# Kernel optimization log

Hardware: AMD Instinct MI355X
Metric: run time of the kernel (lower is better)

The kernel has to match this reference:

```python
import jax, jax.numpy as jnp
import numpy as np

B, H, W, C = 16, 64, 64, 256
NH = 8
KD = C // NH  # 32
SCALE = KD ** -0.5


def rotate_every_two(x):
    x1 = x[..., ::2]
    x2 = x[..., 1::2]
    return jnp.stack([-x2, x1], axis=-1).reshape(x.shape)


def theta_shift(x, sin, cos):
    return x * cos + rotate_every_two(x) * sin


def dwconv2d(x, w, b):
    # x: (b,h,w,c), w: (5,5,1,c) HWIO depthwise, pad 2
    y = jax.lax.conv_general_dilated(
        x, w, window_strides=(1, 1), padding=((2, 2), (2, 2)),
        dimension_numbers=("NHWC", "HWIO", "NHWC"), feature_group_count=x.shape[-1])
    return y + b


def setup_inputs() -> dict:
    key = jax.random.key(0)
    ks = jax.random.split(key, 12)
    s = 0.02
    return {
        "x": jax.random.normal(ks[0], (B, H, W, C), jnp.float32),
        "sin": jax.random.uniform(ks[1], (H, W, KD), jnp.float32, -1.0, 1.0),
        "cos": jax.random.uniform(ks[2], (H, W, KD), jnp.float32, -1.0, 1.0),
        "mask_h": jax.random.normal(ks[3], (NH, H, H), jnp.float32) * 0.1,
        "mask_w": jax.random.normal(ks[4], (NH, W, W), jnp.float32) * 0.1,
        "Wq": jax.random.normal(ks[5], (C, C), jnp.float32) * s,
        "bq": jnp.zeros((C,), jnp.float32),
        "Wk": jax.random.normal(ks[6], (C, C), jnp.float32) * s,
        "bk": jnp.zeros((C,), jnp.float32),
        "Wv": jax.random.normal(ks[7], (C, C), jnp.float32) * s,
        "bv": jnp.zeros((C,), jnp.float32),
        "conv_w": jax.random.normal(ks[8], (5, 5, 1, C), jnp.float32) * s,
        "conv_b": jnp.zeros((C,), jnp.float32),
        "Wo": jax.random.normal(ks[9], (C, C), jnp.float32) * s,
        "bo": jnp.zeros((C,), jnp.float32),
    }


def reference(x, sin, cos, mask_h, mask_w, Wq, bq, Wk, bk, Wv, bv, conv_w, conv_b, Wo, bo):
    b, h, w, _ = x.shape
    n = mask_w.shape[0]
    kd = sin.shape[-1]

    q = x @ Wq + bq
    k = (x @ Wk + bk) * SCALE
    v = x @ Wv + bv
    lepe = dwconv2d(v, conv_w, conv_b)

    # (b,n,h,w,d)
    q = q.reshape(b, h, w, n, kd).transpose(0, 3, 1, 2, 4)
    k = k.reshape(b, h, w, n, kd).transpose(0, 3, 1, 2, 4)
    qr = theta_shift(q, sin, cos)
    kr = theta_shift(k, sin, cos)

    # width attention: rows independent
    qk_w = jnp.einsum("bhnwd,bhnvd->bhnwv", qr.transpose(0, 2, 1, 3, 4), kr.transpose(0, 2, 1, 3, 4))
    qk_w = jax.nn.softmax(qk_w + mask_w, axis=-1)
    vv = v.reshape(b, h, w, n, -1).transpose(0, 1, 3, 2, 4)  # (b,h,n,w,d2)
    vv = jnp.einsum("bhnwv,bhnvd->bhnwd", qk_w, vv)

    # height attention: columns independent
    qr_h = qr.transpose(0, 3, 1, 2, 4)  # (b,w,n,h,d)
    kr_h = kr.transpose(0, 3, 1, 2, 4)
    vv = vv.transpose(0, 3, 2, 1, 4)  # (b,w,n,h,d2)
    qk_h = jnp.einsum("bwnhd,bwngd->bwnhg", qr_h, kr_h)
    qk_h = jax.nn.softmax(qk_h + mask_h, axis=-1)
    out = jnp.einsum("bwnhg,bwngd->bwnhd", qk_h, vv)

    out = out.transpose(0, 3, 1, 2, 4).reshape(b, h, w, -1)  # (b,h,w,n*d2)
    out = out + lepe
    return out @ Wo + bo
```

## Files before the change

### kernel.cpp

```cpp
#include <hip/hip_runtime.h>

typedef __attribute__((ext_vector_type(8))) short bf16x8;
typedef __attribute__((ext_vector_type(4))) float f32x4;

constexpr int B  = 16;
constexpr int H  = 64;
constexpr int W  = 64;
constexpr int C  = 256;
constexpr int NH = 8;
constexpr int KD = 32;
constexpr float SCALE = 0.17677669529663687f;
constexpr int M_TOT = B * H * W;
constexpr size_t NEL = (size_t)B * H * W * C;

__device__ __forceinline__ unsigned short f2bf(float f) {
    union { float f; unsigned int u; } x; x.f = f;
    unsigned int u = x.u;
    unsigned int r = (u + 0x7fffu + ((u >> 16) & 1u)) >> 16;
    return (unsigned short)r;
}
__device__ __forceinline__ float bf2f(unsigned short s) {
    union { unsigned int u; float f; } x; x.u = ((unsigned int)s) << 16; return x.f;
}
__device__ __forceinline__ float bf_lo(unsigned int u) {
    union { unsigned int u; float f; } x; x.u = u << 16; return x.f;
}
__device__ __forceinline__ float bf_hi(unsigned int u) {
    union { unsigned int u; float f; } x; x.u = u & 0xffff0000u; return x.f;
}
__device__ __forceinline__ unsigned int pack2(float a, float b) {
    return (unsigned int)f2bf(a) | ((unsigned int)f2bf(b) << 16);
}
__device__ __forceinline__ void cvt8(uint4 rv, float* f) {
    f[0] = bf_lo(rv.x); f[1] = bf_hi(rv.x); f[2] = bf_lo(rv.y); f[3] = bf_hi(rv.y);
    f[4] = bf_lo(rv.z); f[5] = bf_hi(rv.z); f[6] = bf_lo(rv.w); f[7] = bf_hi(rv.w);
}
__device__ __forceinline__ int swz(int row, int kp8) {
    return row * 32 + (kp8 ^ (((row >> 2) & 3) << 3));
}

typedef const __attribute__((address_space(1))) unsigned int gas_uint;
typedef __attribute__((address_space(3))) unsigned int las_uint;
__device__ __forceinline__ void gl16(const unsigned short* g, unsigned short* l) {
    __builtin_amdgcn_global_load_lds((gas_uint*)g, (las_uint*)l, 16, 0, 0);
}

__global__ __launch_bounds__(256) void prep_x16(const float* __restrict__ x,
                                                unsigned short* __restrict__ x16) {
    size_t i8 = ((size_t)blockIdx.x * 256 + threadIdx.x) * 8;
    float4 f0 = *(const float4*)(x + i8);
    float4 f1 = *(const float4*)(x + i8 + 4);
    uint4 o;
    o.x = pack2(f0.x, f0.y); o.y = pack2(f0.z, f0.w);
    o.z = pack2(f1.x, f1.y); o.w = pack2(f1.z, f1.w);
    *(uint4*)(x16 + i8) = o;
}

__global__ __launch_bounds__(256) void trans_w(const float* __restrict__ src,
                                               unsigned short* __restrict__ dst) {
    int tid = blockIdx.x * 256 + threadIdx.x;
    int n = tid >> 5, k0 = (tid & 31) << 3;
    unsigned int p[4];
#pragma unroll
    for (int j = 0; j < 4; ++j) {
        float a  = src[(size_t)(k0 + 2 * j) * 256 + n];
        float b2 = src[(size_t)(k0 + 2 * j + 1) * 256 + n];
        p[j] = pack2(a, b2);
    }
    uint4 o = {p[0], p[1], p[2], p[3]};
    *(uint4*)(dst + (size_t)n * 256 + k0) = o;
}

template <int QK>
__global__ __launch_bounds__(256) void qkv_part(
    const unsigned short* __restrict__ x16, const unsigned short* __restrict__ Wt16,
    const float* __restrict__ bq, const float* __restrict__ bk, const float* __restrict__ bv,
    const float* __restrict__ sin_t, const float* __restrict__ cos_t,
    unsigned short* __restrict__ qr, unsigned short* __restrict__ kr,
    unsigned short* __restrict__ v16)
{
    __shared__ __align__(16) unsigned short As[2][128 * 32];
    __shared__ __align__(16) unsigned short Bs[2][128 * 32];

    const int t = threadIdx.x;
    const int lane = t & 63, wid = t >> 6;
    const int wr = wid >> 1, wc = wid & 1;
    const int m0 = blockIdx.x * 128;
    const int yb = blockIdx.y;
    const int wrow0 = QK ? yb * 128 : 512 + yb * 128;
    const int nb    = QK ? (yb & 1) * 128 : yb * 128;
    const int matid = QK ? (yb >> 1) : 2;

    f32x4 acc[4][4];
#pragma unroll
    for (int i = 0; i < 4; ++i)
#pragma unroll
        for (int j = 0; j < 4; ++j)
#pragma unroll
            for (int q = 0; q < 4; ++q) acc[i][j][q] = 0.f;

    const int lco = ((lane >> 2) << 8) + (((lane & 3) ^ (lane >> 4)) << 3);
    const unsigned short* ag = x16 + (size_t)m0 * 256 + lco;
    const unsigned short* bg = Wt16 + (size_t)wrow0 * 256 + lco;
    const int lds0 = wid * 16 * 32;
    const int lds1 = (64 + wid * 16) * 32;
    const int rg0 = wid * 16 * 256, rg1 = (64 + wid * 16) * 256;

    const int rsel = lane & 15, kg8 = (lane >> 4) << 3;

    gl16(ag + rg0, &As[0][lds0]);
    gl16(ag + rg1, &As[0][lds1]);
    gl16(bg + rg0, &Bs[0][lds0]);
    gl16(bg + rg1, &Bs[0][lds1]);
    __syncthreads();

    int cur = 0;
    for (int ks = 0; ks < 8; ++ks) {
        if (ks < 7) {
            const int kn = (ks + 1) * 32;
            gl16(ag + rg0 + kn, &As[cur ^ 1][lds0]);
            gl16(ag + rg1 + kn, &As[cur ^ 1][lds1]);
            gl16(bg + rg0 + kn, &Bs[cur ^ 1][lds0]);
            gl16(bg + rg1 + kn, &Bs[cur ^ 1][lds1]);
        }

        bf16x8 af[4], bf[4];
#pragma unroll
        for (int i = 0; i < 4; ++i)
            af[i] = *(const bf16x8*)(&As[cur][swz(wr * 64 + i * 16 + rsel, kg8)]);
#pragma unroll
        for (int j = 0; j < 4; ++j)
            bf[j] = *(const bf16x8*)(&Bs[cur][swz(wc * 64 + j * 16 + rsel, kg8)]);
#pragma unroll
        for (int i = 0; i < 4; ++i)
#pragma unroll
            for (int j = 0; j < 4; ++j) {
                if (QK)
                    acc[i][j] = __builtin_amdgcn_mfma_f32_16x16x32_bf16(bf[j], af[i], acc[i][j], 0, 0, 0);
                else
                    acc[i][j] = __builtin_amdgcn_mfma_f32_16x16x32_bf16(af[i], bf[j], acc[i][j], 0, 0, 0);
            }
        __syncthreads();
        cur ^= 1;
    }

    const int col_l = lane & 15, rowg = (lane >> 4) << 2;
    if (QK == 0) {
#pragma unroll
        for (int i = 0; i < 4; ++i)
#pragma unroll
            for (int j = 0; j < 4; ++j) {
                int nn = nb + wc * 64 + j * 16 + col_l;
                float bias = bv[nn];
#pragma unroll
                for (int r = 0; r < 4; ++r) {
                    int m = m0 + wr * 64 + i * 16 + rowg + r;
                    v16[(size_t)m * 256 + nn] = f2bf(acc[i][j][r] + bias);
                }
            }
    } else {
        const float sc = matid ? SCALE : 1.0f;
        const float* __restrict__ bias = matid ? bk : bq;
        unsigned short* __restrict__ dst = matid ? kr : qr;
#pragma unroll
        for (int i = 0; i < 4; ++i) {
            const int m = m0 + wr * 64 + i * 16 + col_l;
            const int bb = m >> 12, hh = (m >> 6) & 63, ww = m & 63;
            const size_t pixbase = ((size_t)hh * 64 + ww) * 32;
#pragma unroll
            for (int j = 0; j < 4; ++j) {
                const int n = nb + wc * 64 + j * 16 + rowg;
                const int nh = n >> 5, db = n & 31;
                float4 bias4 = *(const float4*)(bias + n);
                float4 cs4 = *(const float4*)(cos_t + pixbase + db);
                float4 sn4 = *(const float4*)(sin_t + pixbase + db);
                float v0 = (acc[i][j][0] + bias4.x) * sc;
                float v1 = (acc[i][j][1] + bias4.y) * sc;
                float v2 = (acc[i][j][2] + bias4.z) * sc;
                float v3 = (acc[i][j][3] + bias4.w) * sc;
                ushort4 o;
                o.x = f2bf(v0 * cs4.x - v1 * sn4.x);
                o.y = f2bf(v1 * cs4.y + v0 * sn4.y);
                o.z = f2bf(v2 * cs4.z - v3 * sn4.z);
                o.w = f2bf(v3 * cs4.w + v2 * sn4.w);
                *(ushort4*)(dst + ((((size_t)bb * 8 + nh) * 64 + hh) * 64 + ww) * 32 + db) = o;
            }
        }
    }
}

__global__ __launch_bounds__(256) void conv_kernel(
    const unsigned short* __restrict__ v, const float* __restrict__ cw,
    const float* __restrict__ cb, unsigned short* __restrict__ lepe)
{
    size_t tid = (size_t)blockIdx.x * 256 + threadIdx.x;
    const int c8 = (int)(tid & 31) << 3;
    const int w0 = ((int)(tid >> 5) & 15) << 2;
    const int h  = (int)(tid >> 9) & 63;
    const int b  = (int)(tid >> 15);

    float acc[4][8];
    {
        float4 cb0 = *(const float4*)(cb + c8);
        float4 cb1 = *(const float4*)(cb + c8 + 4);
#pragma unroll
        for (int o = 0; o < 4; ++o) {
            acc[o][0] = cb0.x; acc[o][1] = cb0.y; acc[o][2] = cb0.z; acc[o][3] = cb0.w;
            acc[o][4] = cb1.x; acc[o][5] = cb1.y; acc[o][6] = cb1.z; acc[o][7] = cb1.w;
        }
    }

    const unsigned short* __restrict__ vb = v + (size_t)b * 4096 * 256 + c8;
#pragma unroll
    for (int dy = 0; dy < 5; ++dy) {
        const int yy = h + dy - 2;
        if (yy < 0 || yy >= 64) continue;
        float rowf[8][8];
#pragma unroll
        for (int j = 0; j < 8; ++j) {
            const int xx = w0 + j - 2;
            if (xx < 0 || xx >= 64) {
#pragma unroll
                for (int q = 0; q < 8; ++q) rowf[j][q] = 0.f;
            } else {
                uint4 rv = *(const uint4*)(vb + (size_t)(yy * 64 + xx) * 256);
                cvt8(rv, rowf[j]);
            }
        }
#pragma unroll
        for (int dx = 0; dx < 5; ++dx) {
            const float* wp = cw + (dy * 5 + dx) * 256 + c8;
            float4 wv0 = *(const float4*)wp;
            float4 wv1 = *(const float4*)(wp + 4);
#pragma unroll
            for (int o = 0; o < 4; ++o) {
                const float* rf = rowf[dx + o];
                acc[o][0] += rf[0] * wv0.x; acc[o][1] += rf[1] * wv0.y;
                acc[o][2] += rf[2] * wv0.z; acc[o][3] += rf[3] * wv0.w;
                acc[o][4] += rf[4] * wv1.x; acc[o][5] += rf[5] * wv1.y;
                acc[o][6] += rf[6] * wv1.z; acc[o][7] += rf[7] * wv1.w;
            }
        }
    }

    unsigned short* __restrict__ op = lepe + (((size_t)(b * 64 + h) * 64) + w0) * 256 + c8;
#pragma unroll
    for (int o = 0; o < 4; ++o) {
        uint4 ov;
        ov.x = pack2(acc[o][0], acc[o][1]); ov.y = pack2(acc[o][2], acc[o][3]);
        ov.z = pack2(acc[o][4], acc[o][5]); ov.w = pack2(acc[o][6], acc[o][7]);
        *(uint4*)(op + (size_t)o * 256) = ov;
    }
}

template <int AXIS>
__global__ __launch_bounds__(256) void attn_mfma(
    const unsigned short* __restrict__ qr, const unsigned short* __restrict__ kr,
    const unsigned short* __restrict__ vin, const float* __restrict__ mask,
    const unsigned short* __restrict__ addin, unsigned short* __restrict__ outp)
{
    __shared__ __align__(16) short qs[64 * 40];
    __shared__ __align__(16) short ks[64 * 40];
    __shared__ __align__(16) short vt[32 * 72];
    __shared__ __align__(16) short P [64 * 72];

    const int t    = threadIdx.x;
    const int lane = t & 63, wv = t >> 6;
    const int bid  = blockIdx.x;
    const int nh   = bid & 7;
    const int pos  = (bid >> 3) & 63;
    const int b    = bid >> 9;

    size_t qbase, vbase;
    int qstride, vstride;
    if (AXIS == 0) {
        qbase   = ((size_t)(b * 8 + nh) * 64 + pos) * 2048;
        qstride = 32;
        vbase   = ((size_t)(b * 64 + pos) * 64) * 256 + nh * 32;
        vstride = 256;
    } else {
        qbase   = ((size_t)(b * 8 + nh) * 64) * 2048 + pos * 32;
        qstride = 2048;
        vbase   = ((size_t)b * 64 * 64) * 256 + pos * 256 + nh * 32;
        vstride = 16384;
    }

    {
        int row = t >> 2, c8 = (t & 3) << 3;
        uint4 rq = *(const uint4*)(qr + qbase + (size_t)row * qstride + c8);
        *(uint4*)(&qs[row * 40 + c8]) = rq;
        uint4 rk = *(const uint4*)(kr + qbase + (size_t)row * qstride + c8);
        *(uint4*)(&ks[row * 40 + c8]) = rk;
        uint4 rv = *(const uint4*)(vin + vbase + (size_t)row * vstride + c8);
        const unsigned short* pv = (const unsigned short*)&rv;
#pragma unroll
        for (int j = 0; j < 8; ++j) vt[(c8 + j) * 72 + row] = pv[j];
    }
    __syncthreads();

    const int rsel = lane & 15;
    const int kg   = (lane >> 4) << 3;
    const int rowg = (lane >> 4) << 2;

    bf16x8 aq = *(const bf16x8*)(&qs[(wv * 16 + rsel) * 40 + kg]);
    f32x4 s[4];
#pragma unroll
    for (int j = 0; j < 4; ++j) {
        f32x4 z = {0.f, 0.f, 0.f, 0.f};
        bf16x8 bk8 = *(const bf16x8*)(&ks[(j * 16 + rsel) * 40 + kg]);
        s[j] = __builtin_amdgcn_mfma_f32_16x16x32_bf16(aq, bk8, z, 0, 0, 0);
    }

    const float* __restrict__ mrow = mask + (size_t)nh * 4096;
#pragma unroll
    for (int r = 0; r < 4; ++r) {
        const int grow = wv * 16 + rowg + r;
#pragma unroll
        for (int j = 0; j < 4; ++j)
            s[j][r] += mrow[grow * 64 + j * 16 + rsel];
        float mx = fmaxf(fmaxf(s[0][r], s[1][r]), fmaxf(s[2][r], s[3][r]));
        mx = fmaxf(mx, __shfl_xor(mx, 1));
        mx = fmaxf(mx, __shfl_xor(mx, 2));
        mx = fmaxf(mx, __shfl_xor(mx, 4));
        mx = fmaxf(mx, __shfl_xor(mx, 8));
        float e0 = __expf(s[0][r] - mx), e1 = __expf(s[1][r] - mx);
        float e2 = __expf(s[2][r] - mx), e3 = __expf(s[3][r] - mx);
        float sum = e0 + e1 + e2 + e3;
        sum += __shfl_xor(sum, 1);
        sum += __shfl_xor(sum, 2);
        sum += __shfl_xor(sum, 4);
        sum += __shfl_xor(sum, 8);
        float inv = 1.0f / sum;
        P[grow * 72 +      rsel] = f2bf(e0 * inv);
        P[grow * 72 + 16 + rsel] = f2bf(e1 * inv);
        P[grow * 72 + 32 + rsel] = f2bf(e2 * inv);
        P[grow * 72 + 48 + rsel] = f2bf(e3 * inv);
    }
    __syncthreads();

    f32x4 o[2];
#pragma unroll
    for (int n = 0; n < 2; ++n)
#pragma unroll
        for (int q = 0; q < 4; ++q) o[n][q] = 0.f;
#pragma unroll
    for (int kk = 0; kk < 2; ++kk) {
        bf16x8 ap = *(const bf16x8*)(&P[(wv * 16 + rsel) * 72 + kk * 32 + kg]);
#pragma unroll
        for (int n = 0; n < 2; ++n) {
            bf16x8 bv8 = *(const bf16x8*)(&vt[(n * 16 + rsel) * 72 + kk * 32 + kg]);
            o[n] = __builtin_amdgcn_mfma_f32_16x16x32_bf16(ap, bv8, o[n], 0, 0, 0);
        }
    }

#pragma unroll
    for (int n = 0; n < 2; ++n)
#pragma unroll
        for (int r = 0; r < 4; ++r) {
            const int grow = wv * 16 + rowg + r;
            size_t oidx = vbase + (size_t)grow * vstride + n * 16 + rsel;
            float val = o[n][r];
            if (AXIS == 1) val += bf2f(addin[oidx]);
            outp[oidx] = f2bf(val);
        }
}

__global__ __launch_bounds__(256) void gemm_out_mfma(
    const unsigned short* __restrict__ y16, const unsigned short* __restrict__ Wot16,
    const float* __restrict__ bo, float* __restrict__ out)
{
    __shared__ __align__(16) unsigned short As[2][128 * 32];
    __shared__ __align__(16) unsigned short Bs[2][128 * 32];

    const int t = threadIdx.x;
    const int lane = t & 63, wid = t >> 6;
    const int wr = wid >> 1, wc = wid & 1;
    const int m0 = blockIdx.x * 128;
    const int n0 = blockIdx.y * 128;

    f32x4 acc[4][4];
#pragma unroll
    for (int i = 0; i < 4; ++i)
#pragma unroll
        for (int j = 0; j < 4; ++j)
#pragma unroll
            for (int q = 0; q < 4; ++q) acc[i][j][q] = 0.f;

    const int lco = ((lane >> 2) << 8) + (((lane & 3) ^ (lane >> 4)) << 3);
    const unsigned short* ag = y16 + (size_t)m0 * 256 + lco;
    const unsigned short* bg = Wot16 + (size_t)n0 * 256 + lco;
    const int lds0 = wid * 16 * 32;
    const int lds1 = (64 + wid * 16) * 32;
    const int rg0 = wid * 16 * 256, rg1 = (64 + wid * 16) * 256;

    const int rsel = lane & 15, kg8 = (lane >> 4) << 3;

    gl16(ag + rg0, &As[0][lds0]);
    gl16(ag + rg1, &As[0][lds1]);
    gl16(bg + rg0, &Bs[0][lds0]);
    gl16(bg + rg1, &Bs[0][lds1]);
    __syncthreads();

    int cur = 0;
    for (int ks = 0; ks < 8; ++ks) {
        if (ks < 7) {
            const int kn = (ks + 1) * 32;
            gl16(ag + rg0 + kn, &As[cur ^ 1][lds0]);
            gl16(ag + rg1 + kn, &As[cur ^ 1][lds1]);
            gl16(bg + rg0 + kn, &Bs[cur ^ 1][lds0]);
            gl16(bg + rg1 + kn, &Bs[cur ^ 1][lds1]);
        }

        bf16x8 af[4], bf[4];
#pragma unroll
        for (int i = 0; i < 4; ++i)
            af[i] = *(const bf16x8*)(&As[cur][swz(wr * 64 + i * 16 + rsel, kg8)]);
#pragma unroll
        for (int j = 0; j < 4; ++j)
            bf[j] = *(const bf16x8*)(&Bs[cur][swz(wc * 64 + j * 16 + rsel, kg8)]);
#pragma unroll
        for (int i = 0; i < 4; ++i)
#pragma unroll
            for (int j = 0; j < 4; ++j)
                acc[i][j] = __builtin_amdgcn_mfma_f32_16x16x32_bf16(af[i], bf[j], acc[i][j], 0, 0, 0);
        __syncthreads();
        cur ^= 1;
    }

    const int col_l = lane & 15, rowg = (lane >> 4) << 2;
#pragma unroll
    for (int i = 0; i < 4; ++i)
#pragma unroll
        for (int j = 0; j < 4; ++j) {
            int nn = n0 + wc * 64 + j * 16 + col_l;
            float bias = bo[nn];
#pragma unroll
            for (int r = 0; r < 4; ++r) {
                int m = m0 + wr * 64 + i * 16 + rowg + r;
                out[(size_t)m * 256 + nn] = acc[i][j][r] + bias;
            }
        }
}

extern "C" void kernel_launch(void* const* d_in, const int* in_sizes, int n_in,
                              void* d_out, int out_size, void* d_ws, size_t ws_size,
                              hipStream_t stream) {
    const float* x      = (const float*)d_in[0];
    const float* sin_t  = (const float*)d_in[1];
    const float* cos_t  = (const float*)d_in[2];
    const float* mask_h = (const float*)d_in[3];
    const float* mask_w = (const float*)d_in[4];
    const float* Wq     = (const float*)d_in[5];
    const float* bq     = (const float*)d_in[6];
    const float* Wk     = (const float*)d_in[7];
    const float* bk     = (const float*)d_in[8];
    const float* Wv     = (const float*)d_in[9];
    const float* bv     = (const float*)d_in[10];
    const float* conv_w = (const float*)d_in[11];
    const float* conv_b = (const float*)d_in[12];
    const float* Wo     = (const float*)d_in[13];
    const float* bo     = (const float*)d_in[14];

    unsigned short* ws    = (unsigned short*)d_ws;
    unsigned short* v16   = ws;
    unsigned short* lepe16= v16 + NEL;
    unsigned short* qr16  = lepe16 + NEL;
    unsigned short* kr16  = qr16 + NEL;
    unsigned short* y16   = kr16 + NEL;
    unsigned short* Wt16  = y16 + NEL;
    unsigned short* Wot16 = Wt16 + 768 * 256;

    unsigned short* vv16 = (unsigned short*)d_out;
    unsigned short* x16  = (unsigned short*)d_out + NEL;

    prep_x16<<<(int)(NEL / 2048), 256, 0, stream>>>(x, x16);
    trans_w<<<32, 256, 0, stream>>>(Wq, Wt16);
    trans_w<<<32, 256, 0, stream>>>(Wk, Wt16 + 256 * 256);
    trans_w<<<32, 256, 0, stream>>>(Wv, Wt16 + 512 * 256);
    trans_w<<<32, 256, 0, stream>>>(Wo, Wot16);

    qkv_part<1><<<dim3(M_TOT / 128, 4), 256, 0, stream>>>(
        x16, Wt16, bq, bk, bv, sin_t, cos_t, qr16, kr16, v16);
    qkv_part<0><<<dim3(M_TOT / 128, 2), 256, 0, stream>>>(
        x16, Wt16, bq, bk, bv, sin_t, cos_t, qr16, kr16, v16);

    conv_kernel<<<(int)(NEL / 32 / 256), 256, 0, stream>>>(v16, conv_w, conv_b, lepe16);

    attn_mfma<0><<<B * H * NH, 256, 0, stream>>>(qr16, kr16, v16, mask_w, nullptr, vv16);

    attn_mfma<1><<<B * W * NH, 256, 0, stream>>>(qr16, kr16, vv16, mask_h, lepe16, y16);

    gemm_out_mfma<<<dim3(M_TOT / 128, 2), 256, 0, stream>>>(y16, Wot16, bo, (float*)d_out);
}
```

Measured before the change: 250.6 us.

## Keep full X row tile in LDS and stream pre-fragmented weights from global

The QKV and output GEMMs now load the whole 128x256 activation tile into LDS once per block and loop over all output column blocks inside one kernel. Weights are pre-packed into MFMA fragment order, so each lane reads its B operand directly from global or L2 without staging it in LDS. This removes the repeated activation reads across grid.y blocks and the per-k-step barriers. In exchange it uses 64KB of LDS per block, which can limit occupancy, and each block does more serial work with fewer blocks in the grid.

Result: slower. 259.5 us (+3.5%).

```diff
diff --git a/kernel.cpp b/kernel.cpp
--- a/kernel.cpp
+++ b/kernel.cpp
@@ -56,10 +56,14 @@
     *(uint4*)(x16 + i8) = o;
 }
 
-__global__ __launch_bounds__(256) void trans_w(const float* __restrict__ src,
-                                               unsigned short* __restrict__ dst) {
+__global__ __launch_bounds__(256) void trans_wf(const float* __restrict__ src,
+                                                unsigned short* __restrict__ dst) {
     int tid = blockIdx.x * 256 + threadIdx.x;
-    int n = tid >> 5, k0 = (tid & 31) << 3;
+    int lane = tid & 63;
+    int ks   = (tid >> 6) & 7;
+    int g    = tid >> 9;
+    int n    = g * 16 + (lane & 15);
+    int k0   = ks * 32 + ((lane >> 4) << 3);
     unsigned int p[4];
 #pragma unroll
     for (int j = 0; j < 4; ++j) {
@@ -68,97 +72,67 @@
         p[j] = pack2(a, b2);
     }
     uint4 o = {p[0], p[1], p[2], p[3]};
-    *(uint4*)(dst + (size_t)n * 256 + k0) = o;
-}
-
-template <int QK>
-__global__ __launch_bounds__(256) void qkv_part(
-    const unsigned short* __restrict__ x16, const unsigned short* __restrict__ Wt16,
+    *(uint4*)(dst + (size_t)tid * 8) = o;
+}
+
+__global__ __launch_bounds__(256) void qkv_fused(
+    const unsigned short* __restrict__ x16, const unsigned short* __restrict__ wf,
     const float* __restrict__ bq, const float* __restrict__ bk, const float* __restrict__ bv,
     const float* __restrict__ sin_t, const float* __restrict__ cos_t,
     unsigned short* __restrict__ qr, unsigned short* __restrict__ kr,
     unsigned short* __restrict__ v16)
 {
-    __shared__ __align__(16) unsigned short As[2][128 * 32];
-    __shared__ __align__(16) unsigned short Bs[2][128 * 32];
+    __shared__ __align__(16) unsigned short xs[8][128 * 32];
 
     const int t = threadIdx.x;
     const int lane = t & 63, wid = t >> 6;
     const int wr = wid >> 1, wc = wid & 1;
     const int m0 = blockIdx.x * 128;
-    const int yb = blockIdx.y;
-    const int wrow0 = QK ? yb * 128 : 512 + yb * 128;
-    const int nb    = QK ? (yb & 1) * 128 : yb * 128;
-    const int matid = QK ? (yb >> 1) : 2;
+    const int rsel = lane & 15, kg8 = (lane >> 4) << 3;
+    const int col_l = lane & 15, rowg = (lane >> 4) << 2;
+
+    const int lco = ((lane >> 2) << 8) + (((lane & 3) ^ (lane >> 4)) << 3);
+    {
+        const unsigned short* ag = x16 + (size_t)m0 * 256 + lco;
+        const int r0 = wid * 16, r1 = 64 + wid * 16;
+#pragma unroll
+        for (int g = 0; g < 8; ++g) {
+            gl16(ag + r0 * 256 + g * 32, &xs[g][r0 * 32]);
+            gl16(ag + r1 * 256 + g * 32, &xs[g][r1 * 32]);
+        }
+    }
+    __syncthreads();
 
     f32x4 acc[4][4];
-#pragma unroll
-    for (int i = 0; i < 4; ++i)
-#pragma unroll
-        for (int j = 0; j < 4; ++j)
-#pragma unroll
-            for (int q = 0; q < 4; ++q) acc[i][j][q] = 0.f;
-
-    const int lco = ((lane >> 2) << 8) + (((lane & 3) ^ (lane >> 4)) << 3);
-    const unsigned short* ag = x16 + (size_t)m0 * 256 + lco;
-    const unsigned short* bg = Wt16 + (size_t)wrow0 * 256 + lco;
-    const int lds0 = wid * 16 * 32;
-    const int lds1 = (64 + wid * 16) * 32;
-    const int rg0 = wid * 16 * 256, rg1 = (64 + wid * 16) * 256;
-
-    const int rsel = lane & 15, kg8 = (lane >> 4) << 3;
-
-    gl16(ag + rg0, &As[0][lds0]);
-    gl16(ag + rg1, &As[0][lds1]);
-    gl16(bg + rg0, &Bs[0][lds0]);
-    gl16(bg + rg1, &Bs[0][lds1]);
-    __syncthreads();
-
-    int cur = 0;
-    for (int ks = 0; ks < 8; ++ks) {
-        if (ks < 7) {
-            const int kn = (ks + 1) * 32;
-            gl16(ag + rg0 + kn, &As[cur ^ 1][lds0]);
-            gl16(ag + rg1 + kn, &As[cur ^ 1][lds1]);
-            gl16(bg + rg0 + kn, &Bs[cur ^ 1][lds0]);
-            gl16(bg + rg1 + kn, &Bs[cur ^ 1][lds1]);
-        }
-
-        bf16x8 af[4], bf[4];
+
+#pragma unroll 1
+    for (int ni = 0; ni < 4; ++ni) {
 #pragma unroll
         for (int i = 0; i < 4; ++i)
-            af[i] = *(const bf16x8*)(&As[cur][swz(wr * 64 + i * 16 + rsel, kg8)]);
-#pragma unroll
-        for (int j = 0; j < 4; ++j)
-            bf[j] = *(const bf16x8*)(&Bs[cur][swz(wc * 64 + j * 16 + rsel, kg8)]);
-#pragma unroll
-        for (int i = 0; i < 4; ++i)
-#pragma unroll
-            for (int j = 0; j < 4; ++j) {
-                if (QK)
+#pragma unroll
+            for (int j = 0; j < 4; ++j)
+#pragma unroll
+                for (int q = 0; q < 4; ++q) acc[i][j][q] = 0.f;
+
+        const int gb = ni * 8 + wc * 4;
+#pragma unroll
+        for (int ks = 0; ks < 8; ++ks) {
+            bf16x8 af[4], bf[4];
+#pragma unroll
+            for (int i = 0; i < 4; ++i)
+                af[i] = *(const bf16x8*)(&xs[ks][swz(wr * 64 + i * 16 + rsel, kg8)]);
+#pragma unroll
+            for (int j = 0; j < 4; ++j)
+                bf[j] = *(const bf16x8*)(wf + (((size_t)(gb + j) * 8 + ks) * 64 + lane) * 8);
+#pragma unroll
+            for (int i = 0; i < 4; ++i)
+#pragma unroll
+                for (int j = 0; j < 4; ++j)
                     acc[i][j] = __builtin_amdgcn_mfma_f32_16x16x32_bf16(bf[j], af[i], acc[i][j], 0, 0, 0);
-                else
-                    acc[i][j] = __builtin_amdgcn_mfma_f32_16x16x32_bf16(af[i], bf[j], acc[i][j], 0, 0, 0);
-            }
-        __syncthreads();
-        cur ^= 1;
-    }
-
-    const int col_l = lane & 15, rowg = (lane >> 4) << 2;
-    if (QK == 0) {
-#pragma unroll
-        for (int i = 0; i < 4; ++i)
-#pragma unroll
-            for (int j = 0; j < 4; ++j) {
-                int nn = nb + wc * 64 + j * 16 + col_l;
-                float bias = bv[nn];
-#pragma unroll
-                for (int r = 0; r < 4; ++r) {
-                    int m = m0 + wr * 64 + i * 16 + rowg + r;
-                    v16[(size_t)m * 256 + nn] = f2bf(acc[i][j][r] + bias);
-                }
-            }
-    } else {
+        }
+
+        const int matid = ni >> 1;
+        const int nb = (ni & 1) * 128;
         const float sc = matid ? SCALE : 1.0f;
         const float* __restrict__ bias = matid ? bk : bq;
         unsigned short* __restrict__ dst = matid ? kr : qr;
@@ -186,6 +160,47 @@
                 *(ushort4*)(dst + ((((size_t)bb * 8 + nh) * 64 + hh) * 64 + ww) * 32 + db) = o;
             }
         }
+    }
+
+#pragma unroll 1
+    for (int ni = 4; ni < 6; ++ni) {
+#pragma unroll
+        for (int i = 0; i < 4; ++i)
+#pragma unroll
+            for (int j = 0; j < 4; ++j)
+#pragma unroll
+                for (int q = 0; q < 4; ++q) acc[i][j][q] = 0.f;
+
+        const int gb = ni * 8 + wc * 4;
+#pragma unroll
+        for (int ks = 0; ks < 8; ++ks) {
+            bf16x8 af[4], bf[4];
+#pragma unroll
+            for (int i = 0; i < 4; ++i)
+                af[i] = *(const bf16x8*)(&xs[ks][swz(wr * 64 + i * 16 + rsel, kg8)]);
+#pragma unroll
+            for (int j = 0; j < 4; ++j)
+                bf[j] = *(const bf16x8*)(wf + (((size_t)(gb + j) * 8 + ks) * 64 + lane) * 8);
+#pragma unroll
+            for (int i = 0; i < 4; ++i)
+#pragma unroll
+                for (int j = 0; j < 4; ++j)
+                    acc[i][j] = __builtin_amdgcn_mfma_f32_16x16x32_bf16(af[i], bf[j], acc[i][j], 0, 0, 0);
+        }
+
+        const int nb = (ni - 4) * 128;
+#pragma unroll
+        for (int i = 0; i < 4; ++i)
+#pragma unroll
+            for (int j = 0; j < 4; ++j) {
+                int nn = nb + wc * 64 + j * 16 + col_l;
+                float bias = bv[nn];
+#pragma unroll
+                for (int r = 0; r < 4; ++r) {
+                    int m = m0 + wr * 64 + i * 16 + rowg + r;
+                    v16[(size_t)m * 256 + nn] = f2bf(acc[i][j][r] + bias);
+                }
+            }
     }
 }
 
@@ -365,81 +380,72 @@
         }
 }
 
-__global__ __launch_bounds__(256) void gemm_out_mfma(
-    const unsigned short* __restrict__ y16, const unsigned short* __restrict__ Wot16,
+__global__ __launch_bounds__(256) void gemm_out_fused(
+    const unsigned short* __restrict__ y16, const unsigned short* __restrict__ wof,
     const float* __restrict__ bo, float* __restrict__ out)
 {
-    __shared__ __align__(16) unsigned short As[2][128 * 32];
-    __shared__ __align__(16) unsigned short Bs[2][128 * 32];
+    __shared__ __align__(16) unsigned short xs[8][128 * 32];
 
     const int t = threadIdx.x;
     const int lane = t & 63, wid = t >> 6;
     const int wr = wid >> 1, wc = wid & 1;
     const int m0 = blockIdx.x * 128;
-    const int n0 = blockIdx.y * 128;
+    const int rsel = lane & 15, kg8 = (lane >> 4) << 3;
+    const int col_l = lane & 15, rowg = (lane >> 4) << 2;
+
+    const int lco = ((lane >> 2) << 8) + (((lane & 3) ^ (lane >> 4)) << 3);
+    {
+        const unsigned short* ag = y16 + (size_t)m0 * 256 + lco;
+        const int r0 = wid * 16, r1 = 64 + wid * 16;
+#pragma unroll
+        for (int g = 0; g < 8; ++g) {
+            gl16(ag + r0 * 256 + g * 32, &xs[g][r0 * 32]);
+            gl16(ag + r1 * 256 + g * 32, &xs[g][r1 * 32]);
+        }
+    }
+    __syncthreads();
 
     f32x4 acc[4][4];
-#pragma unroll
-    for (int i = 0; i < 4; ++i)
-#pragma unroll
-        for (int j = 0; j < 4; ++j)
-#pragma unroll
-            for (int q = 0; q < 4; ++q) acc[i][j][q] = 0.f;
-
-    const int lco = ((lane >> 2) << 8) + (((lane & 3) ^ (lane >> 4)) << 3);
-    const unsigned short* ag = y16 + (size_t)m0 * 256 + lco;
-    const unsigned short* bg = Wot16 + (size_t)n0 * 256 + lco;
-    const int lds0 = wid * 16 * 32;
-    const int lds1 = (64 + wid * 16) * 32;
-    const int rg0 = wid * 16 * 256, rg1 = (64 + wid * 16) * 256;
-
-    const int rsel = lane & 15, kg8 = (lane >> 4) << 3;
-
-    gl16(ag + rg0, &As[0][lds0]);
-    gl16(ag + rg1, &As[0][lds1]);
-    gl16(bg + rg0, &Bs[0][lds0]);
-    gl16(bg + rg1, &Bs[0][lds1]);
-    __syncthreads();
-
-    int cur = 0;
-    for (int ks = 0; ks < 8; ++ks) {
-        if (ks < 7) {
-            const int kn = (ks + 1) * 32;
-            gl16(ag + rg0 + kn, &As[cur ^ 1][lds0]);
-            gl16(ag + rg1 + kn, &As[cur ^ 1][lds1]);
-            gl16(bg + rg0 + kn, &Bs[cur ^ 1][lds0]);
-            gl16(bg + rg1 + kn, &Bs[cur ^ 1][lds1]);
-        }
-
-        bf16x8 af[4], bf[4];
+#pragma unroll 1
+    for (int ni = 0; ni < 2; ++ni) {
 #pragma unroll
         for (int i = 0; i < 4; ++i)
-            af[i] = *(const bf16x8*)(&As[cur][swz(wr * 64 + i * 16 + rsel, kg8)]);
-#pragma unroll
-        for (int j = 0; j < 4; ++j)
-            bf[j] = *(const bf16x8*)(&Bs[cur][swz(wc * 64 + j * 16 + rsel, kg8)]);
+#pragma unroll
+            for (int j = 0; j < 4; ++j)
+#pragma unroll
+                for (int q = 0; q < 4; ++q) acc[i][j][q] = 0.f;
+
+        const int gb = ni * 8 + wc * 4;
+#pragma unroll
+        for (int ks = 0; ks < 8; ++ks) {
+            bf16x8 af[4], bf[4];
+#pragma unroll
+            for (int i = 0; i < 4; ++i)
+                af[i] = *(const bf16x8*)(&xs[ks][swz(wr * 64 + i * 16 + rsel, kg8)]);
+#pragma unroll
+            for (int j = 0; j < 4; ++j)
+                bf[j] = *(const bf16x8*)(wof + (((size_t)(gb + j) * 8 + ks) * 64 + lane) * 8);
+#pragma unroll
+            for (int i = 0; i < 4; ++i)
+#pragma unroll
+                for (int j = 0; j < 4; ++j)
+                    acc[i][j] = __builtin_amdgcn_mfma_f32_16x16x32_bf16(af[i], bf[j], acc[i][j], 0, 0, 0);
+        }
+
+        const int nb = ni * 128;
 #pragma unroll
         for (int i = 0; i < 4; ++i)
 #pragma unroll
-            for (int j = 0; j < 4; ++j)
-                acc[i][j] = __builtin_amdgcn_mfma_f32_16x16x32_bf16(af[i], bf[j], acc[i][j], 0, 0, 0);
-        __syncthreads();
-        cur ^= 1;
-    }
-
-    const int col_l = lane & 15, rowg = (lane >> 4) << 2;
-#pragma unroll
-    for (int i = 0; i < 4; ++i)
-#pragma unroll
-        for (int j = 0; j < 4; ++j) {
-            int nn = n0 + wc * 64 + j * 16 + col_l;
-            float bias = bo[nn];
-#pragma unroll
-            for (int r = 0; r < 4; ++r) {
-                int m = m0 + wr * 64 + i * 16 + rowg + r;
-                out[(size_t)m * 256 + nn] = acc[i][j][r] + bias;
+            for (int j = 0; j < 4; ++j) {
+                int nn = nb + wc * 64 + j * 16 + col_l;
+                float bias = bo[nn];
+#pragma unroll
+                for (int r = 0; r < 4; ++r) {
+                    int m = m0 + wr * 64 + i * 16 + rowg + r;
+                    out[(size_t)m * 256 + nn] = acc[i][j][r] + bias;
+                }
             }
-        }
+    }
 }
 
 extern "C" void kernel_launch(void* const* d_in, const int* in_sizes, int n_in,
@@ -467,22 +473,20 @@
     unsigned short* qr16  = lepe16 + NEL;
     unsigned short* kr16  = qr16 + NEL;
     unsigned short* y16   = kr16 + NEL;
-    unsigned short* Wt16  = y16 + NEL;
-    unsigned short* Wot16 = Wt16 + 768 * 256;
+    unsigned short* wf    = y16 + NEL;
+    unsigned short* wof   = wf + 3 * 65536;
 
     unsigned short* vv16 = (unsigned short*)d_out;
     unsigned short* x16  = (unsigned short*)d_out + NEL;
 
     prep_x16<<<(int)(NEL / 2048), 256, 0, stream>>>(x, x16);
-    trans_w<<<32, 256, 0, stream>>>(Wq, Wt16);
-    trans_w<<<32, 256, 0, stream>>>(Wk, Wt16 + 256 * 256);
-    trans_w<<<32, 256, 0, stream>>>(Wv, Wt16 + 512 * 256);
-    trans_w<<<32, 256, 0, stream>>>(Wo, Wot16);
-
-    qkv_part<1><<<dim3(M_TOT / 128, 4), 256, 0, stream>>>(
-        x16, Wt16, bq, bk, bv, sin_t, cos_t, qr16, kr16, v16);
-    qkv_part<0><<<dim3(M_TOT / 128, 2), 256, 0, stream>>>(
-        x16, Wt16, bq, bk, bv, sin_t, cos_t, qr16, kr16, v16);
+    trans_wf<<<32, 256, 0, stream>>>(Wq, wf);
+    trans_wf<<<32, 256, 0, stream>>>(Wk, wf + 65536);
+    trans_wf<<<32, 256, 0, stream>>>(Wv, wf + 2 * 65536);
+    trans_wf<<<32, 256, 0, stream>>>(Wo, wof);
+
+    qkv_fused<<<M_TOT / 128, 256, 0, stream>>>(
+        x16, wf, bq, bk, bv, sin_t, cos_t, qr16, kr16, v16);
 
     conv_kernel<<<(int)(NEL / 32 / 256), 256, 0, stream>>>(v16, conv_w, conv_b, lepe16);
 
@@ -490,5 +494,5 @@
 
     attn_mfma<1><<<B * W * NH, 256, 0, stream>>>(qr16, kr16, vv16, mask_h, lepe16, y16);
 
-    gemm_out_mfma<<<dim3(M_TOT / 128, 2), 256, 0, stream>>>(y16, Wot16, bo, (float*)d_out);
-}
+    gemm_out_fused<<<M_TOT / 128, 256, 0, stream>>>(y16, wof, bo, (float*)d_out);
+}
```
